# Kernel tuning notes

Measured on AMD Instinct MI355X. Metric: run time of the kernel, lower is better.

Reference implementation:

```python
import jax, jax.numpy as jnp
import numpy as np

B, H, S, E = 1, 32, 2048, 512  # batch, num_heads (also head dim), seq, embed
NEG_INF = -1.0e9


def setup_inputs() -> dict:
    key = jax.random.key(0)
    ks = jax.random.split(key, 9)
    query = jax.random.normal(ks[0], (B, H, S, E), dtype=jnp.float32)
    key_t = jax.random.normal(ks[1], (B, H, S, E), dtype=jnp.float32)
    value = jax.random.normal(ks[2], (B, H, S, E), dtype=jnp.float32)
    mask = jax.random.randint(ks[3], (1, 1, S, S), 0, 2).astype(jnp.bool_)
    # Linear(E -> H) weights, torch layout [out, in]
    lim = 1.0 / np.sqrt(E)
    Wq = jax.random.uniform(ks[4], (H, E), jnp.float32, -lim, lim)
    Wk = jax.random.uniform(ks[5], (H, E), jnp.float32, -lim, lim)
    Wv = jax.random.uniform(ks[6], (H, E), jnp.float32, -lim, lim)
    bq = jnp.zeros((H,), jnp.float32)
    bk = jnp.zeros((H,), jnp.float32)
    bv = jnp.zeros((H,), jnp.float32)
    # learned per-head inverse scale; kept away from 0 (torch init of zeros would divide-by-zero)
    inv_scale = jax.random.uniform(ks[7], (1, H, 1, 1), jnp.float32, 0.5, 1.5)
    return {"query": query, "key": key_t, "value": value, "mask": mask,
            "Wq": Wq, "bq": bq, "Wk": Wk, "bk": bk, "Wv": Wv, "bv": bv,
            "inv_scale": inv_scale}


def reference(query, key, value, mask, Wq, bq, Wk, bk, Wv, bv, inv_scale):
    # projections: [B,H,S,E] @ [E,Hd] -> [B,H,S,Hd] with Hd == num_heads
    q = jnp.einsum('bhse,de->bhsd', query, Wq) + bq
    k = jnp.einsum('bhse,de->bhsd', key, Wk) + bk
    v = jnp.einsum('bhse,de->bhsd', value, Wv) + bv
    qk = jnp.einsum('bhsd,bhtd->bhst', q, k)        # [B,H,S,S]
    scaled = qk / inv_scale                          # learned per-head scale
    masked = jnp.where(mask, NEG_INF, scaled)        # custom mask-fill
    attn = jax.nn.softmax(masked, axis=-1)
    # dropout_p = 0.0 -> identity
    out = jnp.einsum('bhst,bhtd->bhsd', attn, v)     # [B,H,S,Hd]
    return out
```

## Files before the change

kernel.cpp:

```cpp
#include <hip/hip_runtime.h>

#define Hh 32
#define Ss 2048
#define Ee 512
#define Dd 32
#define LOG2E 1.4426950408889634f
#define KV_SPLIT 4
#define KV_LEN (Ss / KV_SPLIT)

typedef __attribute__((ext_vector_type(4))) float f32x4;
typedef __attribute__((ext_vector_type(4))) int i32x4;
typedef __attribute__((ext_vector_type(8))) __bf16 bf16x8;
typedef __attribute__((ext_vector_type(8))) unsigned short ushort8;
typedef __attribute__((ext_vector_type(4))) unsigned short ushort4v;

__device__ inline unsigned short f2bf(float f) {
  union { float f; unsigned u; } x; x.f = f;
  unsigned r = x.u + 0x7fffu + ((x.u >> 16) & 1u);
  return (unsigned short)(r >> 16);
}

__global__ __launch_bounds__(256) void prep_kernel(
    const int* __restrict__ mask, unsigned int* __restrict__ bits,
    const float* __restrict__ Wq, const float* __restrict__ Wk,
    const float* __restrict__ Wv, unsigned short* __restrict__ Wb) {
  int b = (int)blockIdx.x, t = (int)threadIdx.x;
  if (b < 512) {
    int w = b * 256 + t;
    const i32x4* p = (const i32x4*)(mask + (size_t)w * 32);
    unsigned int bs = 0;
    #pragma unroll
    for (int i = 0; i < 8; ++i) {
      i32x4 v = __builtin_nontemporal_load(&p[i]);
      bs |= (v.x ? 1u : 0u) << (4 * i + 0);
      bs |= (v.y ? 1u : 0u) << (4 * i + 1);
      bs |= (v.z ? 1u : 0u) << (4 * i + 2);
      bs |= (v.w ? 1u : 0u) << (4 * i + 3);
    }
    bits[w] = bs;
  } else {
    int i = (b - 512) * 1024 + t * 4;
    const float* src = (i < 16384) ? (Wq + i)
                     : (i < 32768) ? (Wk + (i - 16384)) : (Wv + (i - 32768));
    f32x4 v = *(const f32x4*)src;
    ushort4v o = { f2bf(v.x), f2bf(v.y), f2bf(v.z), f2bf(v.w) };
    *(ushort4v*)(Wb + i) = o;
  }
}

__global__ __launch_bounds__(256) void proj_kernel(
    const float* __restrict__ Xq, const float* __restrict__ Xk,
    const float* __restrict__ Xv, const unsigned short* __restrict__ Wb,
    const float* __restrict__ bq, const float* __restrict__ bk,
    const float* __restrict__ bv, const float* __restrict__ inv_scale,
    unsigned short* __restrict__ Qb, unsigned short* __restrict__ Kb,
    unsigned short* __restrict__ Vtb) {
  __shared__ unsigned short sb[4][2][16 * 64];

  int blk  = (int)blockIdx.x;
  int seg  = blk >> 10;
  int tid  = (int)threadIdx.x;
  int wv   = tid >> 6, lane = tid & 63;
  int g = lane >> 4, li = lane & 15;
  int lr = lane >> 4;
  int lc = lane & 15;
  int R0 = (blk & 1023) * 64;
  int h  = R0 >> 11;
  int s0 = R0 & 2047;

  const float* X    = (seg == 0) ? Xq : (seg == 1) ? Xk : Xv;
  const float* bias = (seg == 0) ? bq : (seg == 1) ? bk : bv;
  const unsigned short* W = Wb + seg * (Dd * Ee);
  const float* xw = X + (size_t)(R0 + wv * 16) * Ee;

  unsigned short (*mybuf)[16 * 64] = sb[wv];

  auto ld = [&](int c, int i) -> f32x4 {
    return __builtin_nontemporal_load(
        (const f32x4*)(xw + (size_t)(4 * i + lr) * Ee + c * 64 + lc * 4));
  };
  auto wr = [&](int buf, int i, f32x4 v) {
    int r = 4 * i + lr;
    int byteoff = (lc * 8) ^ ((r & 7) << 4);
    ushort4v u = { f2bf(v.x), f2bf(v.y), f2bf(v.z), f2bf(v.w) };
    *(ushort4v*)&mybuf[buf][r * 64 + (byteoff >> 1)] = u;
  };
  auto rd = [&](int buf, int half) -> bf16x8 {
    int byteoff = (half * 64 + g * 16) ^ ((li & 7) << 4);
    return __builtin_bit_cast(bf16x8,
        *(const ushort8*)&mybuf[buf][li * 64 + (byteoff >> 1)]);
  };

  f32x4 acc0 = {0.f, 0.f, 0.f, 0.f};
  f32x4 acc1 = {0.f, 0.f, 0.f, 0.f};

  f32x4 A0 = ld(0, 0), A1 = ld(0, 1), A2 = ld(0, 2), A3 = ld(0, 3);
  f32x4 B0 = ld(1, 0), B1 = ld(1, 1), B2 = ld(1, 2), B3 = ld(1, 3);

  #pragma unroll
  for (int c = 0; c < 8; c += 2) {
    wr(0, 0, A0); wr(0, 1, A1); wr(0, 2, A2); wr(0, 3, A3);
    {
      int cn = (c + 2 < 8) ? (c + 2) : 6;
      A0 = ld(cn, 0); A1 = ld(cn, 1); A2 = ld(cn, 2); A3 = ld(cn, 3);
    }
    {
      const unsigned short* wl = W + (size_t)li * Ee + c * 64 + g * 8;
      ushort8 w00 = *(const ushort8*)(wl);
      ushort8 w01 = *(const ushort8*)(wl + 16 * Ee);
      ushort8 w10 = *(const ushort8*)(wl + 32);
      ushort8 w11 = *(const ushort8*)(wl + 16 * Ee + 32);
      bf16x8 a0 = rd(0, 0), a1 = rd(0, 1);
      acc0 = __builtin_amdgcn_mfma_f32_16x16x32_bf16(
          a0, __builtin_bit_cast(bf16x8, w00), acc0, 0, 0, 0);
      acc1 = __builtin_amdgcn_mfma_f32_16x16x32_bf16(
          a0, __builtin_bit_cast(bf16x8, w01), acc1, 0, 0, 0);
      acc0 = __builtin_amdgcn_mfma_f32_16x16x32_bf16(
          a1, __builtin_bit_cast(bf16x8, w10), acc0, 0, 0, 0);
      acc1 = __builtin_amdgcn_mfma_f32_16x16x32_bf16(
          a1, __builtin_bit_cast(bf16x8, w11), acc1, 0, 0, 0);
    }
    wr(1, 0, B0); wr(1, 1, B1); wr(1, 2, B2); wr(1, 3, B3);
    {
      int cn = (c + 3 < 8) ? (c + 3) : 7;
      B0 = ld(cn, 0); B1 = ld(cn, 1); B2 = ld(cn, 2); B3 = ld(cn, 3);
    }
    {
      const unsigned short* wl = W + (size_t)li * Ee + (c + 1) * 64 + g * 8;
      ushort8 w00 = *(const ushort8*)(wl);
      ushort8 w01 = *(const ushort8*)(wl + 16 * Ee);
      ushort8 w10 = *(const ushort8*)(wl + 32);
      ushort8 w11 = *(const ushort8*)(wl + 16 * Ee + 32);
      bf16x8 a0 = rd(1, 0), a1 = rd(1, 1);
      acc0 = __builtin_amdgcn_mfma_f32_16x16x32_bf16(
          a0, __builtin_bit_cast(bf16x8, w00), acc0, 0, 0, 0);
      acc1 = __builtin_amdgcn_mfma_f32_16x16x32_bf16(
          a0, __builtin_bit_cast(bf16x8, w01), acc1, 0, 0, 0);
      acc0 = __builtin_amdgcn_mfma_f32_16x16x32_bf16(
          a1, __builtin_bit_cast(bf16x8, w10), acc0, 0, 0, 0);
      acc1 = __builtin_amdgcn_mfma_f32_16x16x32_bf16(
          a1, __builtin_bit_cast(bf16x8, w11), acc1, 0, 0, 0);
    }
  }

  float blo = bias[li], bhi = bias[li + 16];
  float cs = (seg == 0) ? (LOG2E / inv_scale[h]) : 1.0f;
  int sw = s0 + wv * 16;
  if (seg < 2) {
    unsigned short* ob = ((seg == 0) ? Qb : Kb) +
        (size_t)h * Ss * Dd + (size_t)(sw + 4 * g) * Dd;
    #pragma unroll
    for (int r = 0; r < 4; ++r) {
      ob[r * Dd + li]      = f2bf((acc0[r] + blo) * cs);
      ob[r * Dd + li + 16] = f2bf((acc1[r] + bhi) * cs);
    }
  } else {
    unsigned short* ob = Vtb + (size_t)h * Dd * Ss;
    int s0v = sw + 4 * g;
    int t = s0v >> 5;
    int kkb = 8 * g + ((s0v & 16) ? 4 : 0);
    ushort4v vlo4 = { f2bf(acc0[0] + blo), f2bf(acc0[1] + blo),
                      f2bf(acc0[2] + blo), f2bf(acc0[3] + blo) };
    ushort4v vhi4 = { f2bf(acc1[0] + bhi), f2bf(acc1[1] + bhi),
                      f2bf(acc1[2] + bhi), f2bf(acc1[3] + bhi) };
    *(ushort4v*)&ob[t * 1024 + li * 32 + kkb]        = vlo4;
    *(ushort4v*)&ob[t * 1024 + (li + 16) * 32 + kkb] = vhi4;
  }
}

__global__ __launch_bounds__(256) void attn_kernel(
    const unsigned short* __restrict__ Qb, const unsigned short* __restrict__ Kb,
    const unsigned short* __restrict__ Vt, const unsigned int* __restrict__ mbits,
    float* __restrict__ out) {
  __shared__ float sO[KV_SPLIT][4][8][64];
  __shared__ float sL[KV_SPLIT][4][16];

  int bid  = (int)blockIdx.x;
  int slot = (bid & 7) * 128 + (bid >> 3);
  int w    = (int)threadIdx.x >> 6;
  int lane = (int)threadIdx.x & 63;
  int g = lane >> 4, li = lane & 15;
  int h = slot >> 5, qt = slot & 31;
  int q0 = qt << 6;

  const unsigned short* kb  = Kb + (size_t)h * Ss * Dd;
  const unsigned short* vpb = Vt + (size_t)h * Dd * Ss;
  const unsigned short* qrow = Qb + (size_t)h * Ss * Dd + (size_t)(q0 + li) * Dd + g * 8;
  bf16x8 qfA = __builtin_bit_cast(bf16x8, *(const ushort8*)(qrow));
  bf16x8 qfB = __builtin_bit_cast(bf16x8, *(const ushort8*)(qrow + 16 * Dd));
  bf16x8 qfC = __builtin_bit_cast(bf16x8, *(const ushort8*)(qrow + 32 * Dd));
  bf16x8 qfD = __builtin_bit_cast(bf16x8, *(const ushort8*)(qrow + 48 * Dd));
  const unsigned int* mrowA = mbits + (size_t)(q0 + li) * (Ss / 32);
  const unsigned int* mrowB = mrowA + 16 * (Ss / 32);
  const unsigned int* mrowC = mrowA + 32 * (Ss / 32);
  const unsigned int* mrowD = mrowA + 48 * (Ss / 32);
  const unsigned short* vlo = vpb + li * 32 + 8 * g;
  const unsigned short* vhi = vpb + (li + 16) * 32 + 8 * g;

  ushort8 onesu = { 0x3F80, 0x3F80, 0x3F80, 0x3F80,
                    0x3F80, 0x3F80, 0x3F80, 0x3F80 };
  bf16x8 ones = __builtin_bit_cast(bf16x8, onesu);

  f32x4 oloA = {0.f,0.f,0.f,0.f}, ohiA = {0.f,0.f,0.f,0.f}, lA = {0.f,0.f,0.f,0.f};
  f32x4 oloB = {0.f,0.f,0.f,0.f}, ohiB = {0.f,0.f,0.f,0.f}, lB = {0.f,0.f,0.f,0.f};
  f32x4 oloC = {0.f,0.f,0.f,0.f}, ohiC = {0.f,0.f,0.f,0.f}, lC = {0.f,0.f,0.f,0.f};
  f32x4 oloD = {0.f,0.f,0.f,0.f}, ohiD = {0.f,0.f,0.f,0.f}, lD = {0.f,0.f,0.f,0.f};

  auto seg = [&](f32x4 stx, f32x4 sty, unsigned int msh,
                 f32x4& lacc, f32x4& olo, f32x4& ohi, bf16x8 vl, bf16x8 vh) {
    float p[8];
    #pragma unroll
    for (int r = 0; r < 4; ++r) {
      p[r]     = ((msh >> r) & 1u)        ? 0.f : __builtin_amdgcn_exp2f(stx[r]);
      p[4 + r] = ((msh >> (16 + r)) & 1u) ? 0.f : __builtin_amdgcn_exp2f(sty[r]);
    }
    bf16x8 af;
    #pragma unroll
    for (int j = 0; j < 8; ++j) af[j] = (__bf16)p[j];
    olo  = __builtin_amdgcn_mfma_f32_16x16x32_bf16(af, vl, olo, 0, 0, 0);
    ohi  = __builtin_amdgcn_mfma_f32_16x16x32_bf16(af, vh, ohi, 0, 0, 0);
    lacc = __builtin_amdgcn_mfma_f32_16x16x32_bf16(af, ones, lacc, 0, 0, 0);
  };

  int g4 = 4 * g;
  int kbeg = w * KV_LEN, kend = kbeg + KV_LEN;
  for (int kt = kbeg; kt < kend; kt += 64) {
    bf16x8 k0 = __builtin_bit_cast(bf16x8, *(const ushort8*)(kb + (size_t)(kt      + li) * Dd + g * 8));
    bf16x8 k1 = __builtin_bit_cast(bf16x8, *(const ushort8*)(kb + (size_t)(kt + 16 + li) * Dd + g * 8));
    bf16x8 k2 = __builtin_bit_cast(bf16x8, *(const ushort8*)(kb + (size_t)(kt + 32 + li) * Dd + g * 8));
    bf16x8 k3 = __builtin_bit_cast(bf16x8, *(const ushort8*)(kb + (size_t)(kt + 48 + li) * Dd + g * 8));
    bf16x8 v0lo = __builtin_bit_cast(bf16x8, *(const ushort8*)(vlo + kt * 32));
    bf16x8 v0hi = __builtin_bit_cast(bf16x8, *(const ushort8*)(vhi + kt * 32));
    bf16x8 v1lo = __builtin_bit_cast(bf16x8, *(const ushort8*)(vlo + kt * 32 + 1024));
    bf16x8 v1hi = __builtin_bit_cast(bf16x8, *(const ushort8*)(vhi + kt * 32 + 1024));
    uint2 mwA = *(const uint2*)(mrowA + (kt >> 5));
    uint2 mwB = *(const uint2*)(mrowB + (kt >> 5));
    uint2 mwC = *(const uint2*)(mrowC + (kt >> 5));
    uint2 mwD = *(const uint2*)(mrowD + (kt >> 5));

    f32x4 z = {0.f, 0.f, 0.f, 0.f};
    {
      f32x4 s0 = __builtin_amdgcn_mfma_f32_16x16x32_bf16(k0, qfA, z, 0, 0, 0);
      f32x4 s1 = __builtin_amdgcn_mfma_f32_16x16x32_bf16(k1, qfA, z, 0, 0, 0);
      f32x4 s2 = __builtin_amdgcn_mfma_f32_16x16x32_bf16(k2, qfA, z, 0, 0, 0);
      f32x4 s3 = __builtin_amdgcn_mfma_f32_16x16x32_bf16(k3, qfA, z, 0, 0, 0);
      seg(s0, s1, mwA.x >> g4, lA, oloA, ohiA, v0lo, v0hi);
      seg(s2, s3, mwA.y >> g4, lA, oloA, ohiA, v1lo, v1hi);
    }
    {
      f32x4 s0 = __builtin_amdgcn_mfma_f32_16x16x32_bf16(k0, qfB, z, 0, 0, 0);
      f32x4 s1 = __builtin_amdgcn_mfma_f32_16x16x32_bf16(k1, qfB, z, 0, 0, 0);
      f32x4 s2 = __builtin_amdgcn_mfma_f32_16x16x32_bf16(k2, qfB, z, 0, 0, 0);
      f32x4 s3 = __builtin_amdgcn_mfma_f32_16x16x32_bf16(k3, qfB, z, 0, 0, 0);
      seg(s0, s1, mwB.x >> g4, lB, oloB, ohiB, v0lo, v0hi);
      seg(s2, s3, mwB.y >> g4, lB, oloB, ohiB, v1lo, v1hi);
    }
    {
      f32x4 s0 = __builtin_amdgcn_mfma_f32_16x16x32_bf16(k0, qfC, z, 0, 0, 0);
      f32x4 s1 = __builtin_amdgcn_mfma_f32_16x16x32_bf16(k1, qfC, z, 0, 0, 0);
      f32x4 s2 = __builtin_amdgcn_mfma_f32_16x16x32_bf16(k2, qfC, z, 0, 0, 0);
      f32x4 s3 = __builtin_amdgcn_mfma_f32_16x16x32_bf16(k3, qfC, z, 0, 0, 0);
      seg(s0, s1, mwC.x >> g4, lC, oloC, ohiC, v0lo, v0hi);
      seg(s2, s3, mwC.y >> g4, lC, oloC, ohiC, v1lo, v1hi);
    }
    {
      f32x4 s0 = __builtin_amdgcn_mfma_f32_16x16x32_bf16(k0, qfD, z, 0, 0, 0);
      f32x4 s1 = __builtin_amdgcn_mfma_f32_16x16x32_bf16(k1, qfD, z, 0, 0, 0);
      f32x4 s2 = __builtin_amdgcn_mfma_f32_16x16x32_bf16(k2, qfD, z, 0, 0, 0);
      f32x4 s3 = __builtin_amdgcn_mfma_f32_16x16x32_bf16(k3, qfD, z, 0, 0, 0);
      seg(s0, s1, mwD.x >> g4, lD, oloD, ohiD, v0lo, v0hi);
      seg(s2, s3, mwD.y >> g4, lD, oloD, ohiD, v1lo, v1hi);
    }
  }

  if (li == 0) {
    #pragma unroll
    for (int r = 0; r < 4; ++r) {
      sL[w][0][4 * g + r] = lA[r];
      sL[w][1][4 * g + r] = lB[r];
      sL[w][2][4 * g + r] = lC[r];
      sL[w][3][4 * g + r] = lD[r];
    }
  }
  #pragma unroll
  for (int r = 0; r < 4; ++r) {
    sO[w][0][r][lane]     = oloA[r];
    sO[w][0][4 + r][lane] = ohiA[r];
    sO[w][1][r][lane]     = oloB[r];
    sO[w][1][4 + r][lane] = ohiB[r];
    sO[w][2][r][lane]     = oloC[r];
    sO[w][2][4 + r][lane] = ohiC[r];
    sO[w][3][r][lane]     = oloD[r];
    sO[w][3][4 + r][lane] = ohiD[r];
  }
  __syncthreads();

  {
    int hf = w;
    float* ob = out + (size_t)h * Ss * Dd + (size_t)(q0 + hf * 16) * Dd;
    #pragma unroll
    for (int r = 0; r < 4; ++r) {
      int row = 4 * g + r;
      float den = sL[0][hf][row] + sL[1][hf][row] +
                  sL[2][hf][row] + sL[3][hf][row];
      float nlo = sO[0][hf][r][lane] + sO[1][hf][r][lane] +
                  sO[2][hf][r][lane] + sO[3][hf][r][lane];
      float nhi = sO[0][hf][4 + r][lane] + sO[1][hf][4 + r][lane] +
                  sO[2][hf][4 + r][lane] + sO[3][hf][4 + r][lane];
      float inv = 1.0f / den;
      ob[row * Dd + li]      = nlo * inv;
      ob[row * Dd + li + 16] = nhi * inv;
    }
  }
}

extern "C" void kernel_launch(void* const* d_in, const int* in_sizes, int n_in,
                              void* d_out, int out_size, void* d_ws, size_t ws_size,
                              hipStream_t stream) {
  const float* query = (const float*)d_in[0];
  const float* key   = (const float*)d_in[1];
  const float* value = (const float*)d_in[2];
  const int*   mask  = (const int*)d_in[3];
  const float* Wq = (const float*)d_in[4];
  const float* bq = (const float*)d_in[5];
  const float* Wk = (const float*)d_in[6];
  const float* bk = (const float*)d_in[7];
  const float* Wv = (const float*)d_in[8];
  const float* bv = (const float*)d_in[9];
  const float* inv_scale = (const float*)d_in[10];

  unsigned short* Qb   = (unsigned short*)d_ws;
  unsigned short* Kbuf = Qb + (size_t)Hh * Ss * Dd;
  unsigned short* Vtb  = Kbuf + (size_t)Hh * Ss * Dd;
  unsigned int*   bits = (unsigned int*)(Vtb + (size_t)Hh * Dd * Ss);
  unsigned short* Wb   = (unsigned short*)(bits + (size_t)Ss * Ss / 32);
  float* out = (float*)d_out;

  dim3 blk(256);
  prep_kernel<<<512 + 48, blk, 0, stream>>>(mask, bits, Wq, Wk, Wv, Wb);
  proj_kernel<<<3072, blk, 0, stream>>>(query, key, value, Wb, bq, bk, bv,
                                        inv_scale, Qb, Kbuf, Vtb);
  attn_kernel<<<1024, blk, 0, stream>>>(Qb, Kbuf, Vtb, bits, out);
}
```

Measured before the change: 136.5 us.

## Split KV across eight waves and compute softmax denominator with VALU sums

Doubles the per-block KV split to eight waves (512 threads), so each wave processes a shorter key range. The row-sum MFMA against a ones vector is replaced by scalar adds plus cross-lane shuffles. Partial outputs are combined with LDS atomic adds into a single zeroed buffer instead of per-wave slices. This adds zero-init, an extra barrier, and atomic contention, and raises register pressure per block.

Result: slower. 222.7 us (+63.2%).

```diff
diff --git a/kernel.cpp b/kernel.cpp
--- a/kernel.cpp
+++ b/kernel.cpp
@@ -5,7 +5,7 @@
 #define Ee 512
 #define Dd 32
 #define LOG2E 1.4426950408889634f
-#define KV_SPLIT 4
+#define KV_SPLIT 8
 #define KV_LEN (Ss / KV_SPLIT)
 
 typedef __attribute__((ext_vector_type(4))) float f32x4;
@@ -168,12 +168,12 @@
   }
 }
 
-__global__ __launch_bounds__(256) void attn_kernel(
+__global__ __launch_bounds__(512) void attn_kernel(
     const unsigned short* __restrict__ Qb, const unsigned short* __restrict__ Kb,
     const unsigned short* __restrict__ Vt, const unsigned int* __restrict__ mbits,
     float* __restrict__ out) {
-  __shared__ float sO[KV_SPLIT][4][8][64];
-  __shared__ float sL[KV_SPLIT][4][16];
+  __shared__ float sO[4][8][64];
+  __shared__ float sL[4][16];
 
   int bid  = (int)blockIdx.x;
   int slot = (bid & 7) * 128 + (bid >> 3);
@@ -182,6 +182,14 @@
   int g = lane >> 4, li = lane & 15;
   int h = slot >> 5, qt = slot & 31;
   int q0 = qt << 6;
+
+  {
+    float* z = &sO[0][0][0];
+    int t = (int)threadIdx.x;
+    z[t] = 0.f; z[t + 512] = 0.f; z[t + 1024] = 0.f; z[t + 1536] = 0.f;
+    if (t < 64) (&sL[0][0])[t] = 0.f;
+  }
+  __syncthreads();
 
   const unsigned short* kb  = Kb + (size_t)h * Ss * Dd;
   const unsigned short* vpb = Vt + (size_t)h * Dd * Ss;
@@ -197,29 +205,26 @@
   const unsigned short* vlo = vpb + li * 32 + 8 * g;
   const unsigned short* vhi = vpb + (li + 16) * 32 + 8 * g;
 
-  ushort8 onesu = { 0x3F80, 0x3F80, 0x3F80, 0x3F80,
-                    0x3F80, 0x3F80, 0x3F80, 0x3F80 };
-  bf16x8 ones = __builtin_bit_cast(bf16x8, onesu);
-
-  f32x4 oloA = {0.f,0.f,0.f,0.f}, ohiA = {0.f,0.f,0.f,0.f}, lA = {0.f,0.f,0.f,0.f};
-  f32x4 oloB = {0.f,0.f,0.f,0.f}, ohiB = {0.f,0.f,0.f,0.f}, lB = {0.f,0.f,0.f,0.f};
-  f32x4 oloC = {0.f,0.f,0.f,0.f}, ohiC = {0.f,0.f,0.f,0.f}, lC = {0.f,0.f,0.f,0.f};
-  f32x4 oloD = {0.f,0.f,0.f,0.f}, ohiD = {0.f,0.f,0.f,0.f}, lD = {0.f,0.f,0.f,0.f};
-
-  auto seg = [&](f32x4 stx, f32x4 sty, unsigned int msh,
-                 f32x4& lacc, f32x4& olo, f32x4& ohi, bf16x8 vl, bf16x8 vh) {
+  f32x4 oloA = {0.f,0.f,0.f,0.f}, ohiA = {0.f,0.f,0.f,0.f};
+  f32x4 oloB = {0.f,0.f,0.f,0.f}, ohiB = {0.f,0.f,0.f,0.f};
+  f32x4 oloC = {0.f,0.f,0.f,0.f}, ohiC = {0.f,0.f,0.f,0.f};
+  f32x4 oloD = {0.f,0.f,0.f,0.f}, ohiD = {0.f,0.f,0.f,0.f};
+  float LA = 0.f, LB = 0.f, LC = 0.f, LD = 0.f;
+
+  auto seg = [&](f32x4 stx, f32x4 sty, unsigned int msh, float& Lp,
+                 f32x4& olo, f32x4& ohi, bf16x8 vl, bf16x8 vh) {
     float p[8];
     #pragma unroll
     for (int r = 0; r < 4; ++r) {
       p[r]     = ((msh >> r) & 1u)        ? 0.f : __builtin_amdgcn_exp2f(stx[r]);
       p[4 + r] = ((msh >> (16 + r)) & 1u) ? 0.f : __builtin_amdgcn_exp2f(sty[r]);
     }
+    Lp += ((p[0] + p[1]) + (p[2] + p[3])) + ((p[4] + p[5]) + (p[6] + p[7]));
     bf16x8 af;
     #pragma unroll
     for (int j = 0; j < 8; ++j) af[j] = (__bf16)p[j];
-    olo  = __builtin_amdgcn_mfma_f32_16x16x32_bf16(af, vl, olo, 0, 0, 0);
-    ohi  = __builtin_amdgcn_mfma_f32_16x16x32_bf16(af, vh, ohi, 0, 0, 0);
-    lacc = __builtin_amdgcn_mfma_f32_16x16x32_bf16(af, ones, lacc, 0, 0, 0);
+    olo = __builtin_amdgcn_mfma_f32_16x16x32_bf16(af, vl, olo, 0, 0, 0);
+    ohi = __builtin_amdgcn_mfma_f32_16x16x32_bf16(af, vh, ohi, 0, 0, 0);
   };
 
   int g4 = 4 * g;
@@ -244,72 +249,67 @@
       f32x4 s1 = __builtin_amdgcn_mfma_f32_16x16x32_bf16(k1, qfA, z, 0, 0, 0);
       f32x4 s2 = __builtin_amdgcn_mfma_f32_16x16x32_bf16(k2, qfA, z, 0, 0, 0);
       f32x4 s3 = __builtin_amdgcn_mfma_f32_16x16x32_bf16(k3, qfA, z, 0, 0, 0);
-      seg(s0, s1, mwA.x >> g4, lA, oloA, ohiA, v0lo, v0hi);
-      seg(s2, s3, mwA.y >> g4, lA, oloA, ohiA, v1lo, v1hi);
+      seg(s0, s1, mwA.x >> g4, LA, oloA, ohiA, v0lo, v0hi);
+      seg(s2, s3, mwA.y >> g4, LA, oloA, ohiA, v1lo, v1hi);
     }
     {
       f32x4 s0 = __builtin_amdgcn_mfma_f32_16x16x32_bf16(k0, qfB, z, 0, 0, 0);
       f32x4 s1 = __builtin_amdgcn_mfma_f32_16x16x32_bf16(k1, qfB, z, 0, 0, 0);
       f32x4 s2 = __builtin_amdgcn_mfma_f32_16x16x32_bf16(k2, qfB, z, 0, 0, 0);
       f32x4 s3 = __builtin_amdgcn_mfma_f32_16x16x32_bf16(k3, qfB, z, 0, 0, 0);
-      seg(s0, s1, mwB.x >> g4, lB, oloB, ohiB, v0lo, v0hi);
-      seg(s2, s3, mwB.y >> g4, lB, oloB, ohiB, v1lo, v1hi);
+      seg(s0, s1, mwB.x >> g4, LB, oloB, ohiB, v0lo, v0hi);
+      seg(s2, s3, mwB.y >> g4, LB, oloB, ohiB, v1lo, v1hi);
     }
     {
       f32x4 s0 = __builtin_amdgcn_mfma_f32_16x16x32_bf16(k0, qfC, z, 0, 0, 0);
       f32x4 s1 = __builtin_amdgcn_mfma_f32_16x16x32_bf16(k1, qfC, z, 0, 0, 0);
       f32x4 s2 = __builtin_amdgcn_mfma_f32_16x16x32_bf16(k2, qfC, z, 0, 0, 0);
       f32x4 s3 = __builtin_amdgcn_mfma_f32_16x16x32_bf16(k3, qfC, z, 0, 0, 0);
-      seg(s0, s1, mwC.x >> g4, lC, oloC, ohiC, v0lo, v0hi);
-      seg(s2, s3, mwC.y >> g4, lC, oloC, ohiC, v1lo, v1hi);
+      seg(s0, s1, mwC.x >> g4, LC, oloC, ohiC, v0lo, v0hi);
+      seg(s2, s3, mwC.y >> g4, LC, oloC, ohiC, v1lo, v1hi);
     }
     {
       f32x4 s0 = __builtin_amdgcn_mfma_f32_16x16x32_bf16(k0, qfD, z, 0, 0, 0);
       f32x4 s1 = __builtin_amdgcn_mfma_f32_16x16x32_bf16(k1, qfD, z, 0, 0, 0);
       f32x4 s2 = __builtin_amdgcn_mfma_f32_16x16x32_bf16(k2, qfD, z, 0, 0, 0);
       f32x4 s3 = __builtin_amdgcn_mfma_f32_16x16x32_bf16(k3, qfD, z, 0, 0, 0);
-      seg(s0, s1, mwD.x >> g4, lD, oloD, ohiD, v0lo, v0hi);
-      seg(s2, s3, mwD.y >> g4, lD, oloD, ohiD, v1lo, v1hi);
-    }
-  }
-
-  if (li == 0) {
-    #pragma unroll
-    for (int r = 0; r < 4; ++r) {
-      sL[w][0][4 * g + r] = lA[r];
-      sL[w][1][4 * g + r] = lB[r];
-      sL[w][2][4 * g + r] = lC[r];
-      sL[w][3][4 * g + r] = lD[r];
-    }
-  }
+      seg(s0, s1, mwD.x >> g4, LD, oloD, ohiD, v0lo, v0hi);
+      seg(s2, s3, mwD.y >> g4, LD, oloD, ohiD, v1lo, v1hi);
+    }
+  }
+
+  LA += __shfl_xor(LA, 16); LA += __shfl_xor(LA, 32);
+  LB += __shfl_xor(LB, 16); LB += __shfl_xor(LB, 32);
+  LC += __shfl_xor(LC, 16); LC += __shfl_xor(LC, 32);
+  LD += __shfl_xor(LD, 16); LD += __shfl_xor(LD, 32);
+
   #pragma unroll
   for (int r = 0; r < 4; ++r) {
-    sO[w][0][r][lane]     = oloA[r];
-    sO[w][0][4 + r][lane] = ohiA[r];
-    sO[w][1][r][lane]     = oloB[r];
-    sO[w][1][4 + r][lane] = ohiB[r];
-    sO[w][2][r][lane]     = oloC[r];
-    sO[w][2][4 + r][lane] = ohiC[r];
-    sO[w][3][r][lane]     = oloD[r];
-    sO[w][3][4 + r][lane] = ohiD[r];
+    atomicAdd(&sO[0][r][lane],     oloA[r]);
+    atomicAdd(&sO[0][4 + r][lane], ohiA[r]);
+    atomicAdd(&sO[1][r][lane],     oloB[r]);
+    atomicAdd(&sO[1][4 + r][lane], ohiB[r]);
+    atomicAdd(&sO[2][r][lane],     oloC[r]);
+    atomicAdd(&sO[2][4 + r][lane], ohiC[r]);
+    atomicAdd(&sO[3][r][lane],     oloD[r]);
+    atomicAdd(&sO[3][4 + r][lane], ohiD[r]);
+  }
+  if (lane < 16) {
+    atomicAdd(&sL[0][li], LA);
+    atomicAdd(&sL[1][li], LB);
+    atomicAdd(&sL[2][li], LC);
+    atomicAdd(&sL[3][li], LD);
   }
   __syncthreads();
 
-  {
-    int hf = w;
-    float* ob = out + (size_t)h * Ss * Dd + (size_t)(q0 + hf * 16) * Dd;
+  if (w < 4) {
+    float* ob = out + (size_t)h * Ss * Dd + (size_t)(q0 + w * 16) * Dd;
     #pragma unroll
     for (int r = 0; r < 4; ++r) {
       int row = 4 * g + r;
-      float den = sL[0][hf][row] + sL[1][hf][row] +
-                  sL[2][hf][row] + sL[3][hf][row];
-      float nlo = sO[0][hf][r][lane] + sO[1][hf][r][lane] +
-                  sO[2][hf][r][lane] + sO[3][hf][r][lane];
-      float nhi = sO[0][hf][4 + r][lane] + sO[1][hf][4 + r][lane] +
-                  sO[2][hf][4 + r][lane] + sO[3][hf][4 + r][lane];
-      float inv = 1.0f / den;
-      ob[row * Dd + li]      = nlo * inv;
-      ob[row * Dd + li + 16] = nhi * inv;
+      float inv = 1.0f / sL[w][row];
+      ob[row * Dd + li]      = sO[w][r][lane] * inv;
+      ob[row * Dd + li + 16] = sO[w][4 + r][lane] * inv;
     }
   }
 }
@@ -336,9 +336,8 @@
   unsigned short* Wb   = (unsigned short*)(bits + (size_t)Ss * Ss / 32);
   float* out = (float*)d_out;
 
-  dim3 blk(256);
-  prep_kernel<<<512 + 48, blk, 0, stream>>>(mask, bits, Wq, Wk, Wv, Wb);
-  proj_kernel<<<3072, blk, 0, stream>>>(query, key, value, Wb, bq, bk, bv,
-                                        inv_scale, Qb, Kbuf, Vtb);
-  attn_kernel<<<1024, blk, 0, stream>>>(Qb, Kbuf, Vtb, bits, out);
-}
+  prep_kernel<<<512 + 48, dim3(256), 0, stream>>>(mask, bits, Wq, Wk, Wv, Wb);
+  proj_kernel<<<3072, dim3(256), 0, stream>>>(query, key, value, Wb, bq, bk, bv,
+                                              inv_scale, Qb, Kbuf, Vtb);
+  attn_kernel<<<1024, dim3(512), 0, stream>>>(Qb, Kbuf, Vtb, bits, out);
+}
```
